# Optimization experiments

Measured on AMD Instinct MI355X. Metric: run time of the kernel, lower is better.

Reference implementation:

```python
import jax, jax.numpy as jnp
import numpy as np


def setup_inputs() -> dict:
    key = jax.random.key(0)
    k1, k2 = jax.random.split(key)
    preds = jax.random.normal(k1, (16, 4096, 3), dtype=jnp.float32)
    gts = jax.random.normal(k2, (16, 4096, 3), dtype=jnp.float32)
    return {"preds": preds, "gts": gts}


def _pairwise_sqdist(x, y):
    # x: [B, N1, D], y: [B, N2, D] -> P: [B, N1, N2]
    rx = jnp.sum(x * x, axis=-1)  # [B, N1]
    ry = jnp.sum(y * y, axis=-1)  # [B, N2]
    zz = jnp.einsum("bnd,bmd->bnm", x, y)  # [B, N1, N2]
    return rx[:, :, None] + ry[:, None, :] - 2.0 * zz


def reference(preds, gts):
    # Symmetric Hausdorff distance (squared-dist version) per batch element.
    P = _pairwise_sqdist(preds, gts)  # [B, N1, N2]
    # min over preds (axis 1) for each gt point, then max over gt points
    loss1 = jnp.max(jnp.min(P, axis=1), axis=1)  # [B]
    # min over gts (axis 2) for each pred point, then max over pred points
    loss2 = jnp.max(jnp.min(P, axis=2), axis=1)  # [B]
    return (loss1 + loss2) * 0.5
```

## Files before the change

kernel.cpp:

```cpp
#include <hip/hip_runtime.h>
#include <math.h>


#define NPTS 4096
#define NB 16
#define TPB 256
#define M 8
#define SPLIT 16
#define HT (TPB * M)
#define OC (NPTS / SPLIT)
#define NHT (NPTS / HT)

__global__ __launch_bounds__(TPB) void init_ws_kernel(unsigned int* ws) {
    ws[(size_t)blockIdx.x * TPB + threadIdx.x] = 0x7F800000u;
}

__global__ __launch_bounds__(TPB) void haus_scan_kernel(
        const float* __restrict__ preds, const float* __restrict__ gts,
        unsigned int* __restrict__ wsmin) {
    const int ht  = blockIdx.x & (NHT - 1);
    const int oc  = blockIdx.x >> 1;
    const int b   = blockIdx.y;
    const int dir = blockIdx.z;
    const int t   = threadIdx.x;

    const float* home = (dir == 0) ? gts : preds;
    const float* opp  = (dir == 0) ? preds : gts;
    const float* hb = home + (size_t)b * NPTS * 3;
    const float* ob = opp  + (size_t)b * NPTS * 3;

    __shared__ float4 q[OC];
    {
        const float* src = ob + (size_t)(oc * OC + t) * 3;
        float qx = src[0], qy = src[1], qz = src[2];
        float hq = 0.5f * fmaf(qx, qx, fmaf(qy, qy, qz * qz));
        q[t] = make_float4(qx, qy, qz, hq);
    }

    float px[M], py[M], pz[M], hp[M], best[M];
#pragma unroll
    for (int k = 0; k < M; ++k) {
        int hi = ht * HT + k * TPB + t;
        px[k] = hb[hi * 3 + 0];
        py[k] = hb[hi * 3 + 1];
        pz[k] = hb[hi * 3 + 2];
        hp[k] = 0.5f * fmaf(px[k], px[k], fmaf(py[k], py[k], pz[k] * pz[k]));
        best[k] = INFINITY;
    }

    __syncthreads();

#pragma unroll 4
    for (int j = 0; j < OC; ++j) {
        float4 qq = q[j];
#pragma unroll
        for (int k = 0; k < M; ++k) {
            float acc = fmaf(-px[k], qq.x, qq.w);
            acc = fmaf(-py[k], qq.y, acc);
            acc = fmaf(-pz[k], qq.z, acc);
            best[k] = fminf(best[k], acc);
        }
    }

    unsigned int* slot = wsmin + ((size_t)dir * NB + b) * NPTS + ht * HT;
#pragma unroll
    for (int k = 0; k < M; ++k) {
        float d2 = fmaxf(best[k] + hp[k], 0.0f);
        atomicMin(slot + k * TPB + t, __float_as_uint(d2));
    }
}

__global__ __launch_bounds__(TPB) void haus_final_kernel(
        const unsigned int* __restrict__ wsmin, float* __restrict__ out) {
    const int b = blockIdx.x;
    const int t = threadIdx.x;
    const float4* w0 = (const float4*)(wsmin + ((size_t)0 * NB + b) * NPTS);
    const float4* w1 = (const float4*)(wsmin + ((size_t)1 * NB + b) * NPTS);
    float m1 = -INFINITY, m2 = -INFINITY;
#pragma unroll
    for (int r = 0; r < NPTS / 4 / TPB; ++r) {
        float4 a = w0[r * TPB + t];
        float4 c = w1[r * TPB + t];
        m1 = fmaxf(fmaxf(fmaxf(a.x, a.y), fmaxf(a.z, a.w)), m1);
        m2 = fmaxf(fmaxf(fmaxf(c.x, c.y), fmaxf(c.z, c.w)), m2);
    }
#pragma unroll
    for (int off = 32; off > 0; off >>= 1) {
        m1 = fmaxf(m1, __shfl_down(m1, off, 64));
        m2 = fmaxf(m2, __shfl_down(m2, off, 64));
    }
    __shared__ float s1[4], s2[4];
    if ((t & 63) == 0) { s1[t >> 6] = m1; s2[t >> 6] = m2; }
    __syncthreads();
    if (t == 0) {
        float a = fmaxf(fmaxf(s1[0], s1[1]), fmaxf(s1[2], s1[3]));
        float c = fmaxf(fmaxf(s2[0], s2[1]), fmaxf(s2[2], s2[3]));
        out[b] = a + c;
    }
}

extern "C" void kernel_launch(void* const* d_in, const int* in_sizes, int n_in,
                              void* d_out, int out_size, void* d_ws, size_t ws_size,
                              hipStream_t stream) {
    const float* preds = (const float*)d_in[0];
    const float* gts   = (const float*)d_in[1];
    float* out = (float*)d_out;
    unsigned int* wsmin = (unsigned int*)d_ws;

    init_ws_kernel<<<dim3(2 * NB * NPTS / TPB), dim3(TPB), 0, stream>>>(wsmin);

    haus_scan_kernel<<<dim3(NHT * SPLIT, NB, 2), dim3(TPB), 0, stream>>>(preds, gts, wsmin);

    haus_final_kernel<<<dim3(NB), dim3(TPB), 0, stream>>>(wsmin, out);
}
```

Before: 97.61 us.

## Fuse final max reduction into scan kernel via last-block atomic counters

Removes the separate final reduction kernel: each scan block bumps a per-(dir,batch) counter, and the last block to finish reduces that row's minima and publishes a partial. A second counter picks one block to combine the partials into the output. The self-norm term is now computed after the loop to save registers, and an empty asm barrier keeps the LDS-loaded query values in VGPRs. This saves one kernel launch but adds fences and serialized tail work in the last blocks.

```diff
diff --git a/kernel.cpp b/kernel.cpp
--- a/kernel.cpp
+++ b/kernel.cpp
@@ -10,14 +10,24 @@
 #define HT (TPB * M)
 #define OC (NPTS / SPLIT)
 #define NHT (NPTS / HT)
+#define BLOCKS_PER_DB (NHT * SPLIT)
+
+#define WSMIN_N (2 * NB * NPTS)
+#define CTR1_OFF WSMIN_N
+#define CTR2_OFF (WSMIN_N + 32)
+#define PART_OFF (WSMIN_N + 33)
 
 __global__ __launch_bounds__(TPB) void init_ws_kernel(unsigned int* ws) {
-    ws[(size_t)blockIdx.x * TPB + threadIdx.x] = 0x7F800000u;
+    if (blockIdx.x < WSMIN_N / TPB) {
+        ws[(size_t)blockIdx.x * TPB + threadIdx.x] = 0x7F800000u;
+    } else if (threadIdx.x < 33) {
+        ws[CTR1_OFF + threadIdx.x] = 0u;
+    }
 }
 
 __global__ __launch_bounds__(TPB) void haus_scan_kernel(
         const float* __restrict__ preds, const float* __restrict__ gts,
-        unsigned int* __restrict__ wsmin) {
+        unsigned int* __restrict__ ws, float* __restrict__ out) {
     const int ht  = blockIdx.x & (NHT - 1);
     const int oc  = blockIdx.x >> 1;
     const int b   = blockIdx.y;
@@ -37,14 +47,13 @@
         q[t] = make_float4(qx, qy, qz, hq);
     }
 
-    float px[M], py[M], pz[M], hp[M], best[M];
+    float px[M], py[M], pz[M], best[M];
 #pragma unroll
     for (int k = 0; k < M; ++k) {
         int hi = ht * HT + k * TPB + t;
         px[k] = hb[hi * 3 + 0];
         py[k] = hb[hi * 3 + 1];
         pz[k] = hb[hi * 3 + 2];
-        hp[k] = 0.5f * fmaf(px[k], px[k], fmaf(py[k], py[k], pz[k] * pz[k]));
         best[k] = INFINITY;
     }
 
@@ -52,50 +61,74 @@
 
 #pragma unroll 4
     for (int j = 0; j < OC; ++j) {
-        float4 qq = q[j];
+        float4 q4 = q[j];
+        float qx = q4.x, qy = q4.y, qz = q4.z, qw = q4.w;
+        asm volatile("" : "+v"(qx), "+v"(qy), "+v"(qz), "+v"(qw));
 #pragma unroll
         for (int k = 0; k < M; ++k) {
-            float acc = fmaf(-px[k], qq.x, qq.w);
-            acc = fmaf(-py[k], qq.y, acc);
-            acc = fmaf(-pz[k], qq.z, acc);
+            float acc = fmaf(-px[k], qx, qw);
+            acc = fmaf(-py[k], qy, acc);
+            acc = fmaf(-pz[k], qz, acc);
             best[k] = fminf(best[k], acc);
         }
     }
 
-    unsigned int* slot = wsmin + ((size_t)dir * NB + b) * NPTS + ht * HT;
+    unsigned int* slot = ws + ((size_t)dir * NB + b) * NPTS + ht * HT;
 #pragma unroll
     for (int k = 0; k < M; ++k) {
-        float d2 = fmaxf(best[k] + hp[k], 0.0f);
-        atomicMin(slot + k * TPB + t, __float_as_uint(d2));
+        int hi = ht * HT + k * TPB + t;
+        float hp = 0.5f * fmaf(px[k], px[k], fmaf(py[k], py[k], pz[k] * pz[k]));
+        float d2 = fmaxf(best[k] + hp, 0.0f);
+        atomicMin(slot - ht * HT + hi, __float_as_uint(d2));
     }
-}
 
-__global__ __launch_bounds__(TPB) void haus_final_kernel(
-        const unsigned int* __restrict__ wsmin, float* __restrict__ out) {
-    const int b = blockIdx.x;
-    const int t = threadIdx.x;
-    const float4* w0 = (const float4*)(wsmin + ((size_t)0 * NB + b) * NPTS);
-    const float4* w1 = (const float4*)(wsmin + ((size_t)1 * NB + b) * NPTS);
-    float m1 = -INFINITY, m2 = -INFINITY;
+    __threadfence();
+    __shared__ bool s_last;
+    __syncthreads();
+    if (t == 0) {
+        unsigned old = atomicAdd(&ws[CTR1_OFF + dir * NB + b], 1u);
+        s_last = (old == BLOCKS_PER_DB - 1);
+    }
+    __syncthreads();
+    if (!s_last) return;
+
+    __threadfence();
+    const unsigned int* basep = ws + ((size_t)dir * NB + b) * NPTS;
+    unsigned mx = 0u;
 #pragma unroll
-    for (int r = 0; r < NPTS / 4 / TPB; ++r) {
-        float4 a = w0[r * TPB + t];
-        float4 c = w1[r * TPB + t];
-        m1 = fmaxf(fmaxf(fmaxf(a.x, a.y), fmaxf(a.z, a.w)), m1);
-        m2 = fmaxf(fmaxf(fmaxf(c.x, c.y), fmaxf(c.z, c.w)), m2);
+    for (int r = 0; r < NPTS / TPB; ++r) {
+        unsigned v = __hip_atomic_load(&basep[r * TPB + t], __ATOMIC_RELAXED,
+                                       __HIP_MEMORY_SCOPE_AGENT);
+        mx = mx > v ? mx : v;
     }
 #pragma unroll
     for (int off = 32; off > 0; off >>= 1) {
-        m1 = fmaxf(m1, __shfl_down(m1, off, 64));
-        m2 = fmaxf(m2, __shfl_down(m2, off, 64));
+        unsigned o = (unsigned)__shfl_down((int)mx, off, 64);
+        mx = mx > o ? mx : o;
     }
-    __shared__ float s1[4], s2[4];
-    if ((t & 63) == 0) { s1[t >> 6] = m1; s2[t >> 6] = m2; }
+    __shared__ unsigned sred[4];
+    if ((t & 63) == 0) sred[t >> 6] = mx;
     __syncthreads();
     if (t == 0) {
-        float a = fmaxf(fmaxf(s1[0], s1[1]), fmaxf(s1[2], s1[3]));
-        float c = fmaxf(fmaxf(s2[0], s2[1]), fmaxf(s2[2], s2[3]));
-        out[b] = a + c;
+        unsigned m01 = sred[0] > sred[1] ? sred[0] : sred[1];
+        unsigned m23 = sred[2] > sred[3] ? sred[2] : sred[3];
+        unsigned m = m01 > m23 ? m01 : m23;
+        __hip_atomic_store(&ws[PART_OFF + dir * NB + b], m, __ATOMIC_RELAXED,
+                           __HIP_MEMORY_SCOPE_AGENT);
+        __threadfence();
+        unsigned old2 = atomicAdd(&ws[CTR2_OFF], 1u);
+        s_last = (old2 == 2 * NB - 1);
+    }
+    __syncthreads();
+    if (!s_last) return;
+
+    __threadfence();
+    if (t < NB) {
+        unsigned u0 = __hip_atomic_load(&ws[PART_OFF + 0 * NB + t], __ATOMIC_RELAXED,
+                                        __HIP_MEMORY_SCOPE_AGENT);
+        unsigned u1 = __hip_atomic_load(&ws[PART_OFF + 1 * NB + t], __ATOMIC_RELAXED,
+                                        __HIP_MEMORY_SCOPE_AGENT);
+        out[t] = __uint_as_float(u0) + __uint_as_float(u1);
     }
 }
 
@@ -105,11 +138,10 @@
     const float* preds = (const float*)d_in[0];
     const float* gts   = (const float*)d_in[1];
     float* out = (float*)d_out;
-    unsigned int* wsmin = (unsigned int*)d_ws;
+    unsigned int* ws = (unsigned int*)d_ws;
 
-    init_ws_kernel<<<dim3(2 * NB * NPTS / TPB), dim3(TPB), 0, stream>>>(wsmin);
+    init_ws_kernel<<<dim3(WSMIN_N / TPB + 1), dim3(TPB), 0, stream>>>(ws);
 
-    haus_scan_kernel<<<dim3(NHT * SPLIT, NB, 2), dim3(TPB), 0, stream>>>(preds, gts, wsmin);
-
-    haus_final_kernel<<<dim3(NB), dim3(TPB), 0, stream>>>(wsmin, out);
+    haus_scan_kernel<<<dim3(NHT * SPLIT, NB, 2), dim3(TPB), 0, stream>>>(
+        preds, gts, ws, out);
 }
```

Result: slower. 149.2 us (+52.9%).
